# Kernel tuning notes

Measured on AMD Instinct MI355X. Metric: run time of the kernel, lower is better.

Reference implementation:

```python
import jax, jax.numpy as jnp
import numpy as np

T, B, S = 64, 32, 128
E, Q, H = 512, 512, 256  # src_encoding_size, query_vec_size, hidden_dim


def setup_inputs() -> dict:
    key = jax.random.key(0)
    ks = jax.random.split(key, 9)
    return {
        "src_encodings": jax.random.normal(ks[0], (B, S, E), jnp.float32),
        "src_token_mask": jax.random.randint(ks[1], (B, S), 0, 2).astype(bool),
        "query_vec": jax.random.normal(ks[2], (T, B, Q), jnp.float32),
        # learned params (nn.Linear stores W as (out, in))
        "W_src": jax.random.normal(ks[3], (H, E), jnp.float32) * (1.0 / np.sqrt(E)),
        "b_src": jax.random.normal(ks[4], (H,), jnp.float32) * 0.01,
        "W_q": jax.random.normal(ks[5], (H, Q), jnp.float32) * (1.0 / np.sqrt(Q)),
        "b_q": jax.random.normal(ks[6], (H,), jnp.float32) * 0.01,
        "w2": jax.random.normal(ks[7], (H,), jnp.float32) * (1.0 / np.sqrt(H)),
        "b2": jax.random.normal(ks[8], (), jnp.float32) * 0.01,
    }


def reference(src_encodings, src_token_mask, query_vec, W_src, b_src, W_q, b_q, w2, b2):
    # src projection: (B,S,H); query projection: (T,B,H)
    src_proj = jnp.einsum('bse,he->bsh', src_encodings, W_src) + b_src
    q_proj = jnp.einsum('tbq,hq->tbh', query_vec, W_q) + b_q
    # broadcast add -> tanh: (T,B,S,H)
    h1 = jnp.tanh(src_proj[None, :, :, :] + q_proj[:, :, None, :])
    # hidden -> 1 reduction: (T,B,S)
    h2 = jnp.einsum('tbsh,h->tbs', h1, w2) + b2
    h2 = jnp.where(src_token_mask[None, :, :], -jnp.inf, h2)
    return jax.nn.softmax(h2, axis=-1)
```

## Files before the change

kernel.cpp:

```cpp
#include <hip/hip_runtime.h>
#include <hip/hip_bf16.h>
#include <math.h>


#define TANH_PRESCALE 2.8853900817779268f
#define LOG2E        1.4426950408889634f

typedef __attribute__((ext_vector_type(8))) short short8;
typedef __attribute__((ext_vector_type(4))) float f32x4;

__device__ __forceinline__ float fast_exp2(float x) {
#if __has_builtin(__builtin_amdgcn_exp2f)
    return __builtin_amdgcn_exp2f(x);
#else
    return exp2f(x);
#endif
}
__device__ __forceinline__ float fast_rcp(float x) {
#if __has_builtin(__builtin_amdgcn_rcpf)
    return __builtin_amdgcn_rcpf(x);
#else
    return 1.0f / x;
#endif
}
__device__ __forceinline__ float hi_part(float x) {
    return __uint_as_float(__float_as_uint(x) & 0xffff0000u);
}
__device__ __forceinline__ unsigned pack2(float a, float b) {
    return __builtin_amdgcn_perm(__float_as_uint(b), __float_as_uint(a), 0x07060302u);
}

#define APITCH 72
#define AHI 0
#define ALO (128 * APITCH)
#define WHI (2 * 128 * APITCH)
#define WLO (WHI + 64 * APITCH)
#define LDS_USHORTS (WLO + 64 * APITCH)

__global__ __launch_bounds__(256) void proj_gemm(
    const float* __restrict__ A0, const float* __restrict__ W0,
    const float* __restrict__ bias0, float* __restrict__ C0, int M0,
    const float* __restrict__ A1, const float* __restrict__ W1,
    const float* __restrict__ bias1, float* __restrict__ C1, int M1)
{
    const int z = blockIdx.z;
    const float* __restrict__ A    = z ? A1    : A0;
    const float* __restrict__ W    = z ? W1    : W0;
    const float* __restrict__ bias = z ? bias1 : bias0;
    const int M = z ? M1 : M0;

    const int mb = blockIdx.x, nb = blockIdx.y;
    if (mb * 128 >= M) return;

    __shared__ unsigned short LdsU[LDS_USHORTS];

    const int tid  = threadIdx.x;
    const int lane = tid & 63;
    const int wv   = tid >> 6;
    const int kf4  = tid & 15;
    const int rb   = tid >> 4;
    const int l15  = lane & 15;
    const int q8   = (lane >> 4) * 8;

    f32x4 acc[2][4];
    #pragma unroll
    for (int i = 0; i < 2; ++i)
        #pragma unroll
        for (int j = 0; j < 4; ++j) acc[i][j] = (f32x4){0.f, 0.f, 0.f, 0.f};

    const float* Ab = A + ((size_t)mb * 128) * 512 + kf4 * 4;
    const float* Wb = W + ((size_t)nb * 64)  * 512 + kf4 * 4;

    for (int kt = 0; kt < 512; kt += 64) {
        __syncthreads();
        #pragma unroll
        for (int p = 0; p < 8; ++p) {
            const int row = rb + 16 * p;
            float4 v = *(const float4*)(Ab + (size_t)row * 512 + kt);
            unsigned* dh = (unsigned*)&LdsU[AHI + row * APITCH + kf4 * 4];
            dh[0] = pack2(v.x, v.y);  dh[1] = pack2(v.z, v.w);
            float lx = v.x - hi_part(v.x), ly = v.y - hi_part(v.y);
            float lz = v.z - hi_part(v.z), lw = v.w - hi_part(v.w);
            unsigned* dl = (unsigned*)&LdsU[ALO + row * APITCH + kf4 * 4];
            dl[0] = pack2(lx, ly);    dl[1] = pack2(lz, lw);
        }
        #pragma unroll
        for (int p = 0; p < 4; ++p) {
            const int row = rb + 16 * p;
            float4 v = *(const float4*)(Wb + (size_t)row * 512 + kt);
            unsigned* dh = (unsigned*)&LdsU[WHI + row * APITCH + kf4 * 4];
            dh[0] = pack2(v.x, v.y);  dh[1] = pack2(v.z, v.w);
            float lx = v.x - hi_part(v.x), ly = v.y - hi_part(v.y);
            float lz = v.z - hi_part(v.z), lw = v.w - hi_part(v.w);
            unsigned* dl = (unsigned*)&LdsU[WLO + row * APITCH + kf4 * 4];
            dl[0] = pack2(lx, ly);    dl[1] = pack2(lz, lw);
        }
        __syncthreads();

        #pragma unroll
        for (int kk = 0; kk < 64; kk += 32) {
            short8 ah[2], al[2], wh[4], wl[4];
            #pragma unroll
            for (int mi = 0; mi < 2; ++mi) {
                const int row = wv * 32 + mi * 16 + l15;
                ah[mi] = *(const short8*)&LdsU[AHI + row * APITCH + kk + q8];
                al[mi] = *(const short8*)&LdsU[ALO + row * APITCH + kk + q8];
            }
            #pragma unroll
            for (int ni = 0; ni < 4; ++ni) {
                const int row = ni * 16 + l15;
                wh[ni] = *(const short8*)&LdsU[WHI + row * APITCH + kk + q8];
                wl[ni] = *(const short8*)&LdsU[WLO + row * APITCH + kk + q8];
            }
            #pragma unroll
            for (int mi = 0; mi < 2; ++mi)
                #pragma unroll
                for (int ni = 0; ni < 4; ++ni) {
                    acc[mi][ni] = __builtin_amdgcn_mfma_f32_16x16x32_bf16(
                        ah[mi], wh[ni], acc[mi][ni], 0, 0, 0);
                    acc[mi][ni] = __builtin_amdgcn_mfma_f32_16x16x32_bf16(
                        ah[mi], wl[ni], acc[mi][ni], 0, 0, 0);
                    acc[mi][ni] = __builtin_amdgcn_mfma_f32_16x16x32_bf16(
                        al[mi], wh[ni], acc[mi][ni], 0, 0, 0);
                }
        }
    }

    float bl[4];
    #pragma unroll
    for (int ni = 0; ni < 4; ++ni) bl[ni] = bias[nb * 64 + ni * 16 + l15];

    __syncthreads();
    if (z == 0) {
        float* E = (float*)LdsU;
        #pragma unroll
        for (int mi = 0; mi < 2; ++mi)
            #pragma unroll
            for (int ni = 0; ni < 4; ++ni) {
                const int m = wv * 32 + mi * 16 + (lane >> 4) * 4;
                const int n = ni * 16 + l15;
                #pragma unroll
                for (int r = 0; r < 4; ++r)
                    E[(m + r) * 68 + n] = (acc[mi][ni][r] + bl[ni]) * TANH_PRESCALE;
            }
        __syncthreads();
        #pragma unroll
        for (int p = 0; p < 2; ++p) {
            const int nq = (tid >> 5) + 8 * p;
            #pragma unroll
            for (int j = 0; j < 4; ++j) {
                const int m = (tid & 31) + 32 * j;
                float4 vv = *(const float4*)&E[m * 68 + nq * 4];
                *(float4*)(C0 + ((size_t)(nb * 16 + nq)) * 16384
                              + (size_t)(mb * 128 + m) * 4) = vv;
            }
        }
    } else {
        #pragma unroll
        for (int mi = 0; mi < 2; ++mi)
            #pragma unroll
            for (int ni = 0; ni < 4; ++ni) {
                const int m = mb * 128 + wv * 32 + mi * 16 + (lane >> 4) * 4;
                const int n = nb * 64 + ni * 16 + l15;
                #pragma unroll
                for (int r = 0; r < 4; ++r)
                    C1[(size_t)(m + r) * 256 + n] = (acc[mi][ni][r] + bl[ni]) * TANH_PRESCALE;
            }
    }
}

__global__ __launch_bounds__(256) void attn_score(
    const float* __restrict__ spq, const float* __restrict__ qp,
    const float* __restrict__ w2, const int* __restrict__ mask,
    float* __restrict__ out)
{
    const int b  = blockIdx.x;
    const int tz = blockIdx.y;
    const int tid = threadIdx.x;

    __shared__ float qp_s[4][256];
    __shared__ float w2_s[256];
    __shared__ float h2_s[2][4][128];

    {
        const int tl = tid >> 6, lane = tid & 63;
        const int t = tz * 4 + tl;
        float4 v = *(const float4*)(qp + (size_t)(t * 32 + b) * 256 + lane * 4);
        *(float4*)&qp_s[tl][lane * 4] = v;
        if (tid < 64) {
            float4 wv = *(const float4*)(w2 + tid * 4);
            *(float4*)&w2_s[tid * 4] = wv;
        }
    }
    __syncthreads();

    const int s    = tid & 127;
    const int half = tid >> 7;
    const int hb   = half * 128;
    const float* sq = spq + (size_t)(half * 32) * 16384 + (size_t)(b * 128 + s) * 4;

    float acc0 = 0.f, acc1 = 0.f, acc2 = 0.f, acc3 = 0.f;
    #pragma unroll 4
    for (int hq = 0; hq < 32; ++hq) {
        float4 s4 = *(const float4*)(sq + (size_t)hq * 16384);
        float4 w4 = *(const float4*)&w2_s[hb + hq * 4];
        float4 q0 = *(const float4*)&qp_s[0][hb + hq * 4];
        float4 q1 = *(const float4*)&qp_s[1][hb + hq * 4];
        float4 q2 = *(const float4*)&qp_s[2][hb + hq * 4];
        float4 q3 = *(const float4*)&qp_s[3][hb + hq * 4];
        #define PN_TERM(sj, wj, q0j, q1j, q2j, q3j)                              \
            { float r;                                                           \
              r = fast_rcp(fast_exp2(sj + q0j) + 1.0f); acc0 = fmaf(wj, r, acc0);\
              r = fast_rcp(fast_exp2(sj + q1j) + 1.0f); acc1 = fmaf(wj, r, acc1);\
              r = fast_rcp(fast_exp2(sj + q2j) + 1.0f); acc2 = fmaf(wj, r, acc2);\
              r = fast_rcp(fast_exp2(sj + q3j) + 1.0f); acc3 = fmaf(wj, r, acc3); }
        PN_TERM(s4.x, w4.x, q0.x, q1.x, q2.x, q3.x)
        PN_TERM(s4.y, w4.y, q0.y, q1.y, q2.y, q3.y)
        PN_TERM(s4.z, w4.z, q0.z, q1.z, q2.z, q3.z)
        PN_TERM(s4.w, w4.w, q0.w, q1.w, q2.w, q3.w)
        #undef PN_TERM
    }
    h2_s[half][0][s] = acc0;
    h2_s[half][1][s] = acc1;
    h2_s[half][2][s] = acc2;
    h2_s[half][3][s] = acc3;
    __syncthreads();

    const int wv = tid >> 6, lane = tid & 63;
    float v0 = -2.0f * (h2_s[0][wv][lane]      + h2_s[1][wv][lane]);
    float v1 = -2.0f * (h2_s[0][wv][lane + 64] + h2_s[1][wv][lane + 64]);
    if (mask[b * 128 + lane])      v0 = -__builtin_inff();
    if (mask[b * 128 + lane + 64]) v1 = -__builtin_inff();

    float mx = fmaxf(v0, v1);
    #pragma unroll
    for (int off = 32; off >= 1; off >>= 1) mx = fmaxf(mx, __shfl_xor(mx, off));
    float e0 = fast_exp2((v0 - mx) * LOG2E);
    float e1 = fast_exp2((v1 - mx) * LOG2E);
    float sum = e0 + e1;
    #pragma unroll
    for (int off = 32; off >= 1; off >>= 1) sum += __shfl_xor(sum, off);
    const float r = fast_rcp(sum);

    const size_t ob = (size_t)((tz * 4 + wv) * 32 + b) * 128;
    out[ob + lane]      = e0 * r;
    out[ob + lane + 64] = e1 * r;
}

extern "C" void kernel_launch(void* const* d_in, const int* in_sizes, int n_in,
                              void* d_out, int out_size, void* d_ws, size_t ws_size,
                              hipStream_t stream) {
    const float* src   = (const float*)d_in[0];
    const int*   mask  = (const int*)  d_in[1];
    const float* query = (const float*)d_in[2];
    const float* W_src = (const float*)d_in[3];
    const float* b_src = (const float*)d_in[4];
    const float* W_q   = (const float*)d_in[5];
    const float* b_q   = (const float*)d_in[6];
    const float* w2    = (const float*)d_in[7];
    float* out = (float*)d_out;

    float* spq = (float*)d_ws;
    float* qp  = spq + 4096 * 256;

    dim3 gA(32, 4, 2);
    proj_gemm<<<gA, 256, 0, stream>>>(src,   W_src, b_src, spq, 4096,
                                      query, W_q,   b_q,   qp,  2048);

    dim3 gB(32, 16);
    attn_score<<<gB, 256, 0, stream>>>(spq, qp, w2, mask, out);
}
```

Measured before the change: 107.9 us.

## Pre-split inputs to bf16 hi/lo, async-load GEMM tiles, widen attention block

A new conversion kernel writes the fp32 activations and weights once as concatenated bf16 hi/lo rows in workspace. The projection GEMM then streams these rows into swizzled, double-buffered LDS tiles with global_load_lds async copies, runs 24 K-stages (hi·hi, hi·lo, lo·hi) at 128 threads with a 64-row-per-wave tile, and no longer converts inside the main loop. The attention kernel moves to 512 threads that split H four ways and reduce through shared memory. The cost is an extra kernel launch and extra workspace traffic for the converted copies, traded for less ALU work and better latency hiding in the GEMM.

```diff
diff --git a/kernel.cpp b/kernel.cpp
--- a/kernel.cpp
+++ b/kernel.cpp
@@ -29,100 +29,121 @@
 __device__ __forceinline__ unsigned pack2(float a, float b) {
     return __builtin_amdgcn_perm(__float_as_uint(b), __float_as_uint(a), 0x07060302u);
 }
-
-#define APITCH 72
-#define AHI 0
-#define ALO (128 * APITCH)
-#define WHI (2 * 128 * APITCH)
-#define WLO (WHI + 64 * APITCH)
-#define LDS_USHORTS (WLO + 64 * APITCH)
-
-__global__ __launch_bounds__(256) void proj_gemm(
-    const float* __restrict__ A0, const float* __restrict__ W0,
-    const float* __restrict__ bias0, float* __restrict__ C0, int M0,
-    const float* __restrict__ A1, const float* __restrict__ W1,
-    const float* __restrict__ bias1, float* __restrict__ C1, int M1)
+__device__ __forceinline__ void async16(const void* g, void* l) {
+    __builtin_amdgcn_global_load_lds(
+        (const __attribute__((address_space(1))) unsigned int*)(unsigned long long)g,
+        (__attribute__((address_space(3))) unsigned int*)(unsigned int)(unsigned long long)l,
+        16, 0, 0);
+}
+
+__global__ __launch_bounds__(256) void convert_hilo(
+    const float* __restrict__ src, const float* __restrict__ query,
+    const float* __restrict__ Wsrc, const float* __restrict__ Wq,
+    unsigned short* __restrict__ Ah, unsigned short* __restrict__ Wsh,
+    unsigned short* __restrict__ Wqh)
 {
-    const int z = blockIdx.z;
-    const float* __restrict__ A    = z ? A1    : A0;
-    const float* __restrict__ W    = z ? W1    : W0;
-    const float* __restrict__ bias = z ? bias1 : bias0;
-    const int M = z ? M1 : M0;
-
-    const int mb = blockIdx.x, nb = blockIdx.y;
-    if (mb * 128 >= M) return;
-
-    __shared__ unsigned short LdsU[LDS_USHORTS];
+    const int b = blockIdx.x;
+    const float* in; unsigned short* out; int r0;
+    if (b < 512)      { in = src;   out = Ah;                      r0 = b * 8; }
+    else if (b < 768) { in = query; out = Ah + (size_t)4096 * 1024; r0 = (b - 512) * 8; }
+    else if (b < 800) { in = Wsrc;  out = Wsh;                     r0 = (b - 768) * 8; }
+    else              { in = Wq;    out = Wqh;                     r0 = (b - 800) * 8; }
+    in  += (size_t)r0 * 512;
+    out += (size_t)r0 * 1024;
+    const int tid = threadIdx.x;
+    #pragma unroll
+    for (int i = 0; i < 4; ++i) {
+        const int idx = i * 256 + tid;
+        const int row = idx >> 7, k4 = idx & 127;
+        float4 v = *(const float4*)(in + (size_t)row * 512 + k4 * 4);
+        unsigned h0 = pack2(v.x, v.y), h1 = pack2(v.z, v.w);
+        float lx = v.x - hi_part(v.x), ly = v.y - hi_part(v.y);
+        float lz = v.z - hi_part(v.z), lw = v.w - hi_part(v.w);
+        unsigned l0 = pack2(lx, ly), l1 = pack2(lz, lw);
+        *(uint2*)(out + (size_t)row * 1024 + k4 * 4)       = make_uint2(h0, h1);
+        *(uint2*)(out + (size_t)row * 1024 + 512 + k4 * 4) = make_uint2(l0, l1);
+    }
+}
+
+__global__ __launch_bounds__(128) void proj_gemm(
+    const unsigned short* __restrict__ Ah,
+    const unsigned short* __restrict__ Wsh, const unsigned short* __restrict__ Wqh,
+    const float* __restrict__ b_src, const float* __restrict__ b_q,
+    float* __restrict__ spq, float* __restrict__ qp)
+{
+    const int bx = blockIdx.x;
+    const int nb = blockIdx.y;
+    const bool isSrc = bx < 32;
+    const int mrow0 = isSrc ? bx * 128 : (bx - 32) * 128;
+    const size_t arow0 = isSrc ? (size_t)bx * 128
+                               : (size_t)4096 + (size_t)(bx - 32) * 128;
+    const unsigned short* Wm = isSrc ? Wsh : Wqh;
+    const float* bias = isSrc ? b_src : b_q;
+
+    __shared__ char LB[49152];
 
     const int tid  = threadIdx.x;
     const int lane = tid & 63;
     const int wv   = tid >> 6;
-    const int kf4  = tid & 15;
-    const int rb   = tid >> 4;
     const int l15  = lane & 15;
-    const int q8   = (lane >> 4) * 8;
-
-    f32x4 acc[2][4];
-    #pragma unroll
-    for (int i = 0; i < 2; ++i)
+    const int l4q  = lane >> 4;
+
+    const int srow = lane >> 3;
+    const int ssw  = (lane & 7) ^ (srow & 7);
+    const size_t g_lane = (size_t)srow * 2048 + (size_t)ssw * 16;
+    const char* Agbase = (const char*)(Ah + arow0 * 1024);
+    const char* Wgbase = (const char*)(Wm + (size_t)(nb * 64) * 1024);
+
+    f32x4 acc[4][4];
+    #pragma unroll
+    for (int i = 0; i < 4; ++i)
         #pragma unroll
         for (int j = 0; j < 4; ++j) acc[i][j] = (f32x4){0.f, 0.f, 0.f, 0.f};
 
-    const float* Ab = A + ((size_t)mb * 128) * 512 + kf4 * 4;
-    const float* Wb = W + ((size_t)nb * 64)  * 512 + kf4 * 4;
-
-    for (int kt = 0; kt < 512; kt += 64) {
+    #define STAGE(p, buf) {                                                     \
+        const int t_  = ((p) < 16) ? ((p) >> 1) : ((p) - 16);                   \
+        const int ka_ = ((p) < 16) ? t_ * 64 : 512 + t_ * 64;                   \
+        const int kw_ = ((p) < 16) ? (((p) & 1) ? 512 + t_ * 64 : t_ * 64)      \
+                                   : t_ * 64;                                   \
+        const char* ag = Agbase + (size_t)ka_ * 2 + g_lane;                     \
+        char* al = LB + (buf) * 16384 + (wv * 64) * 128 + lane * 16;            \
+        _Pragma("unroll")                                                       \
+        for (int i_ = 0; i_ < 8; ++i_)                                          \
+            async16(ag + (size_t)(wv * 64 + i_ * 8) * 2048, al + i_ * 1024);    \
+        const char* wg = Wgbase + (size_t)kw_ * 2 + g_lane;                     \
+        char* wl = LB + 32768 + (buf) * 8192 + (wv * 32) * 128 + lane * 16;     \
+        _Pragma("unroll")                                                       \
+        for (int i_ = 0; i_ < 4; ++i_)                                          \
+            async16(wg + (size_t)(wv * 32 + i_ * 8) * 2048, wl + i_ * 1024);    \
+    }
+
+    STAGE(0, 0)
+    for (int p = 0; p < 24; ++p) {
         __syncthreads();
-        #pragma unroll
-        for (int p = 0; p < 8; ++p) {
-            const int row = rb + 16 * p;
-            float4 v = *(const float4*)(Ab + (size_t)row * 512 + kt);
-            unsigned* dh = (unsigned*)&LdsU[AHI + row * APITCH + kf4 * 4];
-            dh[0] = pack2(v.x, v.y);  dh[1] = pack2(v.z, v.w);
-            float lx = v.x - hi_part(v.x), ly = v.y - hi_part(v.y);
-            float lz = v.z - hi_part(v.z), lw = v.w - hi_part(v.w);
-            unsigned* dl = (unsigned*)&LdsU[ALO + row * APITCH + kf4 * 4];
-            dl[0] = pack2(lx, ly);    dl[1] = pack2(lz, lw);
-        }
-        #pragma unroll
-        for (int p = 0; p < 4; ++p) {
-            const int row = rb + 16 * p;
-            float4 v = *(const float4*)(Wb + (size_t)row * 512 + kt);
-            unsigned* dh = (unsigned*)&LdsU[WHI + row * APITCH + kf4 * 4];
-            dh[0] = pack2(v.x, v.y);  dh[1] = pack2(v.z, v.w);
-            float lx = v.x - hi_part(v.x), ly = v.y - hi_part(v.y);
-            float lz = v.z - hi_part(v.z), lw = v.w - hi_part(v.w);
-            unsigned* dl = (unsigned*)&LdsU[WLO + row * APITCH + kf4 * 4];
-            dl[0] = pack2(lx, ly);    dl[1] = pack2(lz, lw);
-        }
-        __syncthreads();
-
-        #pragma unroll
-        for (int kk = 0; kk < 64; kk += 32) {
-            short8 ah[2], al[2], wh[4], wl[4];
-            #pragma unroll
-            for (int mi = 0; mi < 2; ++mi) {
-                const int row = wv * 32 + mi * 16 + l15;
-                ah[mi] = *(const short8*)&LdsU[AHI + row * APITCH + kk + q8];
-                al[mi] = *(const short8*)&LdsU[ALO + row * APITCH + kk + q8];
+        if (p + 1 < 24) STAGE(p + 1, (p + 1) & 1)
+        const char* At = LB + (p & 1) * 16384;
+        const char* Wt = LB + 32768 + (p & 1) * 8192;
+        #pragma unroll
+        for (int kk = 0; kk < 2; ++kk) {
+            short8 af[4], wf[4];
+            #pragma unroll
+            for (int mi = 0; mi < 4; ++mi) {
+                const int r = wv * 64 + mi * 16 + l15;
+                const int j = (kk * 4 + l4q) ^ (r & 7);
+                af[mi] = *(const short8*)(At + r * 128 + j * 16);
             }
             #pragma unroll
             for (int ni = 0; ni < 4; ++ni) {
-                const int row = ni * 16 + l15;
-                wh[ni] = *(const short8*)&LdsU[WHI + row * APITCH + kk + q8];
-                wl[ni] = *(const short8*)&LdsU[WLO + row * APITCH + kk + q8];
+                const int r = ni * 16 + l15;
+                const int j = (kk * 4 + l4q) ^ (r & 7);
+                wf[ni] = *(const short8*)(Wt + r * 128 + j * 16);
             }
             #pragma unroll
-            for (int mi = 0; mi < 2; ++mi)
+            for (int mi = 0; mi < 4; ++mi)
                 #pragma unroll
-                for (int ni = 0; ni < 4; ++ni) {
+                for (int ni = 0; ni < 4; ++ni)
                     acc[mi][ni] = __builtin_amdgcn_mfma_f32_16x16x32_bf16(
-                        ah[mi], wh[ni], acc[mi][ni], 0, 0, 0);
-                    acc[mi][ni] = __builtin_amdgcn_mfma_f32_16x16x32_bf16(
-                        ah[mi], wl[ni], acc[mi][ni], 0, 0, 0);
-                    acc[mi][ni] = __builtin_amdgcn_mfma_f32_16x16x32_bf16(
-                        al[mi], wh[ni], acc[mi][ni], 0, 0, 0);
-                }
+                        af[mi], wf[ni], acc[mi][ni], 0, 0, 0);
         }
     }
 
@@ -131,45 +152,43 @@
     for (int ni = 0; ni < 4; ++ni) bl[ni] = bias[nb * 64 + ni * 16 + l15];
 
     __syncthreads();
-    if (z == 0) {
-        float* E = (float*)LdsU;
-        #pragma unroll
-        for (int mi = 0; mi < 2; ++mi)
-            #pragma unroll
-            for (int ni = 0; ni < 4; ++ni) {
-                const int m = wv * 32 + mi * 16 + (lane >> 4) * 4;
-                const int n = ni * 16 + l15;
-                #pragma unroll
-                for (int r = 0; r < 4; ++r)
-                    E[(m + r) * 68 + n] = (acc[mi][ni][r] + bl[ni]) * TANH_PRESCALE;
-            }
-        __syncthreads();
-        #pragma unroll
-        for (int p = 0; p < 2; ++p) {
-            const int nq = (tid >> 5) + 8 * p;
+    float* E = (float*)LB;
+    #pragma unroll
+    for (int mi = 0; mi < 4; ++mi)
+        #pragma unroll
+        for (int ni = 0; ni < 4; ++ni) {
+            const int m = wv * 64 + mi * 16 + l4q * 4;
+            const int n = ni * 16 + l15;
+            #pragma unroll
+            for (int r = 0; r < 4; ++r)
+                E[(m + r) * 68 + n] = (acc[mi][ni][r] + bl[ni]) * TANH_PRESCALE;
+        }
+    __syncthreads();
+
+    if (isSrc) {
+        #pragma unroll
+        for (int p2 = 0; p2 < 4; ++p2) {
+            const int nq = (tid >> 5) + 4 * p2;
             #pragma unroll
             for (int j = 0; j < 4; ++j) {
                 const int m = (tid & 31) + 32 * j;
-                float4 vv = *(const float4*)&E[m * 68 + nq * 4];
-                *(float4*)(C0 + ((size_t)(nb * 16 + nq)) * 16384
-                              + (size_t)(mb * 128 + m) * 4) = vv;
+                float4 v = *(const float4*)&E[m * 68 + nq * 4];
+                *(float4*)(spq + (size_t)(nb * 16 + nq) * 16384
+                               + (size_t)(mrow0 + m) * 4) = v;
             }
         }
     } else {
         #pragma unroll
-        for (int mi = 0; mi < 2; ++mi)
-            #pragma unroll
-            for (int ni = 0; ni < 4; ++ni) {
-                const int m = mb * 128 + wv * 32 + mi * 16 + (lane >> 4) * 4;
-                const int n = nb * 64 + ni * 16 + l15;
-                #pragma unroll
-                for (int r = 0; r < 4; ++r)
-                    C1[(size_t)(m + r) * 256 + n] = (acc[mi][ni][r] + bl[ni]) * TANH_PRESCALE;
-            }
-    }
-}
-
-__global__ __launch_bounds__(256) void attn_score(
+        for (int it = 0; it < 16; ++it) {
+            const int m = (tid >> 4) + 8 * it;
+            const int n4 = tid & 15;
+            float4 v = *(const float4*)&E[m * 68 + n4 * 4];
+            *(float4*)(qp + (size_t)(mrow0 + m) * 256 + nb * 64 + n4 * 4) = v;
+        }
+    }
+}
+
+__global__ __launch_bounds__(512) void attn_score(
     const float* __restrict__ spq, const float* __restrict__ qp,
     const float* __restrict__ w2, const int* __restrict__ mask,
     float* __restrict__ out)
@@ -180,28 +199,27 @@
 
     __shared__ float qp_s[4][256];
     __shared__ float w2_s[256];
-    __shared__ float h2_s[2][4][128];
-
-    {
+    __shared__ float h2p[4][4][128];
+
+    if (tid < 256) {
         const int tl = tid >> 6, lane = tid & 63;
         const int t = tz * 4 + tl;
-        float4 v = *(const float4*)(qp + (size_t)(t * 32 + b) * 256 + lane * 4);
-        *(float4*)&qp_s[tl][lane * 4] = v;
-        if (tid < 64) {
-            float4 wv = *(const float4*)(w2 + tid * 4);
-            *(float4*)&w2_s[tid * 4] = wv;
-        }
-    }
-    __syncthreads();
-
-    const int s    = tid & 127;
-    const int half = tid >> 7;
-    const int hb   = half * 128;
-    const float* sq = spq + (size_t)(half * 32) * 16384 + (size_t)(b * 128 + s) * 4;
+        *(float4*)&qp_s[tl][lane * 4] =
+            *(const float4*)(qp + (size_t)(t * 32 + b) * 256 + lane * 4);
+    } else if (tid < 320) {
+        const int i = tid - 256;
+        *(float4*)&w2_s[i * 4] = *(const float4*)(w2 + i * 4);
+    }
+    __syncthreads();
+
+    const int s = tid & 127;
+    const int g = tid >> 7;
+    const int hb = g * 64;
+    const float* sq = spq + (size_t)(g * 16) * 16384 + (size_t)(b * 128 + s) * 4;
 
     float acc0 = 0.f, acc1 = 0.f, acc2 = 0.f, acc3 = 0.f;
     #pragma unroll 4
-    for (int hq = 0; hq < 32; ++hq) {
+    for (int hq = 0; hq < 16; ++hq) {
         float4 s4 = *(const float4*)(sq + (size_t)hq * 16384);
         float4 w4 = *(const float4*)&w2_s[hb + hq * 4];
         float4 q0 = *(const float4*)&qp_s[0][hb + hq * 4];
@@ -220,31 +238,35 @@
         PN_TERM(s4.w, w4.w, q0.w, q1.w, q2.w, q3.w)
         #undef PN_TERM
     }
-    h2_s[half][0][s] = acc0;
-    h2_s[half][1][s] = acc1;
-    h2_s[half][2][s] = acc2;
-    h2_s[half][3][s] = acc3;
-    __syncthreads();
-
-    const int wv = tid >> 6, lane = tid & 63;
-    float v0 = -2.0f * (h2_s[0][wv][lane]      + h2_s[1][wv][lane]);
-    float v1 = -2.0f * (h2_s[0][wv][lane + 64] + h2_s[1][wv][lane + 64]);
-    if (mask[b * 128 + lane])      v0 = -__builtin_inff();
-    if (mask[b * 128 + lane + 64]) v1 = -__builtin_inff();
-
-    float mx = fmaxf(v0, v1);
-    #pragma unroll
-    for (int off = 32; off >= 1; off >>= 1) mx = fmaxf(mx, __shfl_xor(mx, off));
-    float e0 = fast_exp2((v0 - mx) * LOG2E);
-    float e1 = fast_exp2((v1 - mx) * LOG2E);
-    float sum = e0 + e1;
-    #pragma unroll
-    for (int off = 32; off >= 1; off >>= 1) sum += __shfl_xor(sum, off);
-    const float r = fast_rcp(sum);
-
-    const size_t ob = (size_t)((tz * 4 + wv) * 32 + b) * 128;
-    out[ob + lane]      = e0 * r;
-    out[ob + lane + 64] = e1 * r;
+    h2p[g][0][s] = acc0;
+    h2p[g][1][s] = acc1;
+    h2p[g][2][s] = acc2;
+    h2p[g][3][s] = acc3;
+    __syncthreads();
+
+    if (tid < 256) {
+        const int wv = tid >> 6, lane = tid & 63;
+        float v0 = -2.0f * (h2p[0][wv][lane] + h2p[1][wv][lane]
+                          + h2p[2][wv][lane] + h2p[3][wv][lane]);
+        float v1 = -2.0f * (h2p[0][wv][lane + 64] + h2p[1][wv][lane + 64]
+                          + h2p[2][wv][lane + 64] + h2p[3][wv][lane + 64]);
+        if (mask[b * 128 + lane])      v0 = -__builtin_inff();
+        if (mask[b * 128 + lane + 64]) v1 = -__builtin_inff();
+
+        float mx = fmaxf(v0, v1);
+        #pragma unroll
+        for (int off = 32; off >= 1; off >>= 1) mx = fmaxf(mx, __shfl_xor(mx, off));
+        float e0 = fast_exp2((v0 - mx) * LOG2E);
+        float e1 = fast_exp2((v1 - mx) * LOG2E);
+        float sum = e0 + e1;
+        #pragma unroll
+        for (int off = 32; off >= 1; off >>= 1) sum += __shfl_xor(sum, off);
+        const float r = fast_rcp(sum);
+
+        const size_t ob = (size_t)((tz * 4 + wv) * 32 + b) * 128;
+        out[ob + lane]      = e0 * r;
+        out[ob + lane + 64] = e1 * r;
+    }
 }
 
 extern "C" void kernel_launch(void* const* d_in, const int* in_sizes, int n_in,
@@ -261,12 +283,12 @@
     float* out = (float*)d_out;
 
     float* spq = (float*)d_ws;
-    float* qp  = spq + 4096 * 256;
-
-    dim3 gA(32, 4, 2);
-    proj_gemm<<<gA, 256, 0, stream>>>(src,   W_src, b_src, spq, 4096,
-                                      query, W_q,   b_q,   qp,  2048);
-
-    dim3 gB(32, 16);
-    attn_score<<<gB, 256, 0, stream>>>(spq, qp, w2, mask, out);
-}
+    float* qp  = (float*)((char*)d_ws + (4u << 20));
+    unsigned short* Ah  = (unsigned short*)((char*)d_ws + (6u << 20));
+    unsigned short* Wsh = (unsigned short*)((char*)d_ws + 18874368u);
+    unsigned short* Wqh = (unsigned short*)((char*)d_ws + 19398656u);
+
+    convert_hilo<<<832, 256, 0, stream>>>(src, query, W_src, W_q, Ah, Wsh, Wqh);
+    proj_gemm<<<dim3(48, 4), 128, 0, stream>>>(Ah, Wsh, Wqh, b_src, b_q, spq, qp);
+    attn_score<<<dim3(32, 16), 512, 0, stream>>>(spq, qp, w2, mask, out);
+}
```

Result: slower. 116.5 us (+8.0%).
